# Kernel optimization log

Hardware: AMD Instinct MI355X
Metric: run time of the kernel (lower is better)

## Reference

```python
import jax, jax.numpy as jnp
import numpy as np

N, E, G = 50000, 200000, 2000        # nodes, directed edges, graphs in batch
F_IN, HID, HEADS = 64, 128, 4
DM = HID * HEADS                      # 512, concat GAT output dim
EPS = 1e-5
NEG_SLOPE = 0.2                       # PyG GATConv LeakyReLU slope


def setup_inputs() -> dict:
    key = jax.random.key(0)
    ks = jax.random.split(key, 40)
    rn = lambda k, s, sc: jax.random.normal(k, s, jnp.float32) * sc
    inp = {}
    inp["x"] = rn(ks[0], (N, F_IN), 1.0)
    inp["edge_index"] = jax.random.randint(ks[1], (2, E), 0, N)
    inp["batch"] = jnp.sort(jax.random.randint(ks[2], (N,), 0, G))
    dims = [F_IN, DM, DM]
    for l in range(3):
        d = dims[l]
        inp["W%d" % l] = rn(ks[3 + 4 * l], (d, DM), 1.0 / np.sqrt(d))
        inp["as%d" % l] = rn(ks[4 + 4 * l], (HEADS, HID), 0.1)
        inp["ad%d" % l] = rn(ks[5 + 4 * l], (HEADS, HID), 0.1)
        inp["b%d" % l] = jnp.zeros((DM,), jnp.float32)
        inp["g%d" % l] = jnp.ones((DM,), jnp.float32)
        inp["be%d" % l] = jnp.zeros((DM,), jnp.float32)
    inp["c1w"] = rn(ks[20], (2 * DM, HID), 1.0 / np.sqrt(2 * DM))
    inp["c1b"] = jnp.zeros((HID,), jnp.float32)
    inp["c2w"] = rn(ks[21], (HID, HID // 2), 1.0 / np.sqrt(HID))
    inp["c2b"] = jnp.zeros((HID // 2,), jnp.float32)
    inp["c3w"] = rn(ks[22], (HID // 2, 1), 1.0 / np.sqrt(HID // 2))
    inp["c3b"] = jnp.zeros((1,), jnp.float32)
    return inp


def _gat(x, src, dst, W, a_s, a_d, b):
    """PyG GATConv (heads=HEADS, concat) with self-loops already in src/dst."""
    n = x.shape[0]
    h = (x @ W).reshape(n, HEADS, HID)                     # [N,H,D]
    s_src = jnp.sum(h * a_s, -1)                           # [N,H]
    s_dst = jnp.sum(h * a_d, -1)                           # [N,H]
    e = jax.nn.leaky_relu(s_src[src] + s_dst[dst], NEG_SLOPE)  # [Et,H]
    # segment softmax over incoming edges of each dst node (stable)
    m = jax.lax.stop_gradient(jax.ops.segment_max(e, dst, num_segments=n))
    ex = jnp.exp(e - m[dst])
    alpha = ex / jax.ops.segment_sum(ex, dst, num_segments=n)[dst]
    out = jax.ops.segment_sum(h[src] * alpha[:, :, None], dst, num_segments=n)
    return out.reshape(n, HEADS * HID) + b


def _bn(x, g, b):
    mu = jnp.mean(x, 0)
    var = jnp.var(x, 0)
    return (x - mu) * jax.lax.rsqrt(var + EPS) * g + b


def _forward(x, edge_index, batch, layers, c1w, c1b, c2w, c2b, c3w, c3b):
    loops = jnp.arange(N)
    src = jnp.concatenate([edge_index[0], loops])          # add self-loops
    dst = jnp.concatenate([edge_index[1], loops])
    for (W, a_s, a_d, b, g, be) in layers:
        x = jax.nn.relu(_bn(_gat(x, src, dst, W, a_s, a_d, b), g, be))
    cnt = jax.ops.segment_sum(jnp.ones((N,), x.dtype), batch, num_segments=G)
    mean = jax.ops.segment_sum(x, batch, num_segments=G) / jnp.maximum(cnt, 1.0)[:, None]
    mx = jax.ops.segment_max(x, batch, num_segments=G)
    mx = jnp.where(cnt[:, None] > 0, mx, 0.0)
    h = jnp.concatenate([mean, mx], 1)                     # [G, 2*DM]
    h = jax.nn.relu(h @ c1w + c1b)
    h = jax.nn.relu(h @ c2w + c2b)
    return jax.nn.sigmoid(h @ c3w + c3b).squeeze(-1)       # [G]


def reference(x, edge_index, batch, W0, as0, ad0, b0, g0, be0, W1, as1, ad1, b1, g1, be1, W2, as2, ad2, b2, g2, be2, c1w, c1b, c2w, c2b, c3w, c3b):
    layers = [(W0, as0, ad0, b0, g0, be0), (W1, as1, ad1, b1, g1, be1), (W2, as2, ad2, b2, g2, be2)]
    return _forward(x, edge_index, batch, layers, c1w, c1b, c2w, c2b, c3w, c3b)
```

## Files before the change

kernel.cpp:

```cpp
#include <hip/hip_runtime.h>

#define N_NODES 50000
#define E_EDGES 200000
#define ET_EDGES (E_EDGES + N_NODES)
#define G_GRAPHS 2000
#define F_IN 64
#define HID 128
#define HEADS 4
#define DM 512
#define BN_EPS 1e-5f
#define NEG_SLOPE 0.2f
#define YBLK 391
#define NCHUNK (YBLK / 8)

typedef unsigned short ushort_t;
typedef float floatx4 __attribute__((ext_vector_type(4)));
typedef short short8 __attribute__((ext_vector_type(8)));

__device__ __forceinline__ float b2f(unsigned int u) {
    union { unsigned int i; float f; } v; v.i = u << 16; return v.f;
}
__device__ __forceinline__ ushort_t f2b(float f) {
    union { float f; unsigned int i; } v; v.f = f;
    unsigned int r = v.i + 0x7FFFu + ((v.i >> 16) & 1u);
    return (ushort_t)(r >> 16);
}
__device__ __forceinline__ void unpack8(uint4 v, float* f) {
    f[0] = b2f(v.x & 0xffffu); f[1] = b2f(v.x >> 16);
    f[2] = b2f(v.y & 0xffffu); f[3] = b2f(v.y >> 16);
    f[4] = b2f(v.z & 0xffffu); f[5] = b2f(v.z >> 16);
    f[6] = b2f(v.w & 0xffffu); f[7] = b2f(v.w >> 16);
}
__device__ __forceinline__ void glds16(const ushort_t* g, ushort_t* l) {
    __builtin_amdgcn_global_load_lds(
        (const __attribute__((address_space(1))) unsigned int*)g,
        (__attribute__((address_space(3))) unsigned int*)l, 16, 0, 0);
}

#define XN (N_NODES * F_IN)
#define W0N (F_IN * DM)
#define W1N (DM * DM)
__global__ __launch_bounds__(256) void k_prep(const float* __restrict__ x,
                                              const float* __restrict__ w0,
                                              const float* __restrict__ w1,
                                              const float* __restrict__ w2,
                                              ushort_t* __restrict__ Xb,
                                              ushort_t* __restrict__ Wh0,
                                              ushort_t* __restrict__ Wh1,
                                              ushort_t* __restrict__ Wh2) {
    int t = blockIdx.x * 256 + threadIdx.x;
    if (t < XN) { Xb[t] = f2b(x[t]); return; }
    t -= XN;
    if (t < W0N) {
        int k = t >> 9, n = t & 511;
        Wh0[(size_t)n * F_IN + k] = f2b(w0[t]);
        return;
    }
    t -= W0N;
    if (t < W1N) {
        int k = t >> 9, n = t & 511;
        Wh1[(size_t)n * DM + k] = f2b(w1[t]);
        return;
    }
    t -= W1N;
    if (t < W1N) {
        int k = t >> 9, n = t & 511;
        Wh2[(size_t)n * DM + k] = f2b(w2[t]);
    }
}

__global__ __launch_bounds__(256) void k_mgemm(const ushort_t* __restrict__ A,
                                               const ushort_t* __restrict__ Bh,
                                               const float* __restrict__ a_s,
                                               const float* __restrict__ a_d,
                                               ushort_t* __restrict__ C,
                                               float* __restrict__ ssrc,
                                               float* __restrict__ sdst,
                                               int M, int K) {
    __shared__ __align__(16) ushort_t Ash[128 * 32];
    __shared__ __align__(16) ushort_t Bsh[128 * 32];
    __shared__ float sS[128], sD[128];
    int bid = blockIdx.x;
    int head, yb;
    if (bid < NCHUNK * 32) {
        int chunk = bid >> 5, pos = bid & 31;
        yb = chunk * 8 + (pos & 7);
        head = pos >> 3;
    } else {
        int rem = bid - NCHUNK * 32;
        head = rem & 3;
        yb = NCHUNK * 8 + (rem >> 2);
    }
    int m0 = yb * 128, n0 = head * 128;
    int tid = threadIdx.x;
    int lane = tid & 63, wave = tid >> 6;
    int wm = (wave >> 1) * 64, wn = (wave & 1) * 64;
    floatx4 acc[4][4] = {};
    if (tid < 128) { sS[tid] = 0.f; sD[tid] = 0.f; }
    int lrow = lane >> 2, lchunk = lane & 3;
    int fs = (lrow & 3) ^ ((lrow >> 2) & 3);
    int schunk = lchunk ^ fs;
    int ar0 = wave * 16 + lrow;
    int ar1 = ar0 + 64;
    int gr0 = m0 + ar0; if (gr0 >= M) gr0 = M - 1;
    int gr1 = m0 + ar1; if (gr1 >= M) gr1 = M - 1;
    const ushort_t* gA0 = A + (size_t)gr0 * K + schunk * 8;
    const ushort_t* gA1 = A + (size_t)gr1 * K + schunk * 8;
    const ushort_t* gB0 = Bh + (size_t)(n0 + ar0) * K + schunk * 8;
    const ushort_t* gB1 = Bh + (size_t)(n0 + ar1) * K + schunk * 8;
    ushort_t* lA0 = &Ash[(wave * 16) * 32];
    ushort_t* lA1 = &Ash[(wave * 16 + 64) * 32];
    ushort_t* lB0 = &Bsh[(wave * 16) * 32];
    ushort_t* lB1 = &Bsh[(wave * 16 + 64) * 32];
    int rF = lane & 15, q = lane >> 4;
    int swz = ((q ^ (rF & 3) ^ ((rF >> 2) & 3))) * 8;
    for (int k0 = 0; k0 < K; k0 += 32) {
        glds16(gA0 + k0, lA0);
        glds16(gA1 + k0, lA1);
        glds16(gB0 + k0, lB0);
        glds16(gB1 + k0, lB1);
        __syncthreads();
        short8 af[4], bf[4];
#pragma unroll
        for (int i = 0; i < 4; ++i)
            af[i] = *(const short8*)&Ash[(wm + i * 16 + rF) * 32 + swz];
#pragma unroll
        for (int j = 0; j < 4; ++j)
            bf[j] = *(const short8*)&Bsh[(wn + j * 16 + rF) * 32 + swz];
#pragma unroll
        for (int i = 0; i < 4; ++i)
#pragma unroll
            for (int j = 0; j < 4; ++j)
                acc[i][j] = __builtin_amdgcn_mfma_f32_16x16x32_bf16(af[i], bf[j], acc[i][j], 0, 0, 0);
        __syncthreads();
    }
    int cr = (lane >> 4) * 4, cc = lane & 15;
#pragma unroll
    for (int i = 0; i < 4; ++i) {
#pragma unroll
        for (int r = 0; r < 4; ++r) {
            int gr = m0 + wm + i * 16 + cr + r;
            if (gr < M) {
#pragma unroll
                for (int j = 0; j < 4; ++j)
                    C[(size_t)gr * DM + n0 + wn + j * 16 + cc] = f2b(acc[i][j][r]);
            }
        }
    }
    float asl_[4], adl_[4];
#pragma unroll
    for (int j = 0; j < 4; ++j) {
        int c = wn + j * 16 + cc;
        asl_[j] = a_s[head * HID + c];
        adl_[j] = a_d[head * HID + c];
    }
#pragma unroll
    for (int i = 0; i < 4; ++i) {
#pragma unroll
        for (int r = 0; r < 4; ++r) {
            float ps = 0.f, pd = 0.f;
#pragma unroll
            for (int j = 0; j < 4; ++j) {
                ps += acc[i][j][r] * asl_[j];
                pd += acc[i][j][r] * adl_[j];
            }
#pragma unroll
            for (int mk = 1; mk < 16; mk <<= 1) {
                ps += __shfl_xor(ps, mk);
                pd += __shfl_xor(pd, mk);
            }
            if (cc == 0) {
                int row = wm + i * 16 + (lane >> 4) * 4 + r;
                atomicAdd(&sS[row], ps);
                atomicAdd(&sD[row], pd);
            }
        }
    }
    __syncthreads();
    if (tid < 128) {
        int gr = m0 + tid;
        if (gr < M) {
            ssrc[gr * 4 + head] = sS[tid];
            sdst[gr * 4 + head] = sD[tid];
        }
    }
}

__global__ __launch_bounds__(256) void k_bnapply(const ushort_t* __restrict__ X,
                                                 const float* __restrict__ stat,
                                                 const float* __restrict__ gam,
                                                 const float* __restrict__ bet,
                                                 ushort_t* __restrict__ Y) {
    __shared__ float sc[512], sh[512];
    int t = threadIdx.x;
    for (int f = t; f < 512; f += 256) {
        float mu = stat[f] * (1.f / (float)N_NODES);
        float var = fmaxf(stat[512 + f] * (1.f / (float)N_NODES) - mu * mu, 0.f);
        float rs = rsqrtf(var + BN_EPS);
        float s = gam[f] * rs;
        sc[f] = s;
        sh[f] = bet[f] - mu * s;
    }
    __syncthreads();
    int c8 = (t & 63) * 8;
    const float* scp = sc + c8;
    const float* shp = sh + c8;
    for (int n = blockIdx.x * 4 + (t >> 6); n < N_NODES; n += gridDim.x * 4) {
        uint4 v = *(const uint4*)&X[(size_t)n * DM + c8];
        float fv[8]; unpack8(v, fv);
        uint4 ov; unsigned* po = (unsigned*)&ov;
#pragma unroll
        for (int j = 0; j < 4; ++j) {
            unsigned lo = f2b(fmaxf(fv[2 * j] * scp[2 * j] + shp[2 * j], 0.f));
            unsigned hi = f2b(fmaxf(fv[2 * j + 1] * scp[2 * j + 1] + shp[2 * j + 1], 0.f));
            po[j] = lo | (hi << 16);
        }
        *(uint4*)&Y[(size_t)n * DM + c8] = ov;
    }
}

__global__ void k_degree(const int* __restrict__ ei, int* __restrict__ deg) {
    int e = blockIdx.x * blockDim.x + threadIdx.x;
    if (e >= ET_EDGES) return;
    int d = (e < E_EDGES) ? ei[E_EDGES + e] : (e - E_EDGES);
    atomicAdd(&deg[d], 1);
}

__global__ __launch_bounds__(1024) void k_scan3(const int* __restrict__ deg,
                                                int* __restrict__ offs,
                                                int* __restrict__ cursor) {
    __shared__ int wsum[16];
    __shared__ int carry;
    int t = threadIdx.x;
    int lane = t & 63, wv = t >> 6;
    if (t == 0) carry = 0;
    __syncthreads();
    for (int base = 0; base < N_NODES; base += 1024) {
        int i = base + t;
        int v = (i < N_NODES) ? deg[i] : 0;
        int x = v;
#pragma unroll
        for (int off = 1; off < 64; off <<= 1) {
            int y = __shfl_up(x, off);
            if (lane >= off) x += y;
        }
        if (lane == 63) wsum[wv] = x;
        __syncthreads();
        int wpre = 0;
#pragma unroll
        for (int w = 0; w < 16; ++w) wpre += (w < wv) ? wsum[w] : 0;
        int incl = wpre + x;
        if (i < N_NODES) { int o = carry + (incl - v); offs[i] = o; cursor[i] = o; }
        __syncthreads();
        if (t == 1023) carry += incl;
        __syncthreads();
    }
    if (t == 0) offs[N_NODES] = carry;
}

__global__ void k_scatter(const int* __restrict__ ei, int* __restrict__ cursor,
                          int* __restrict__ csr_src) {
    int e = blockIdx.x * blockDim.x + threadIdx.x;
    if (e >= ET_EDGES) return;
    int sv, d;
    if (e < E_EDGES) { sv = ei[e]; d = ei[E_EDGES + e]; } else { sv = d = e - E_EDGES; }
    int pos = atomicAdd(&cursor[d], 1);
    csr_src[pos] = sv;
}

__global__ void k_gbounds(const int* __restrict__ batch, int* __restrict__ gstart) {
    int i = blockIdx.x * blockDim.x + threadIdx.x;
    if (i >= N_NODES) return;
    int b = batch[i];
    int p = (i == 0) ? -1 : batch[i - 1];
    for (int g = p + 1; g <= b; ++g) gstart[g] = i;
    if (i == N_NODES - 1)
        for (int g = b + 1; g <= G_GRAPHS; ++g) gstart[g] = N_NODES;
}

__global__ __launch_bounds__(256) void k_aggregate(const ushort_t* __restrict__ H,
                                                   const float* __restrict__ ssrc,
                                                   const float* __restrict__ sdst,
                                                   const int* __restrict__ offs,
                                                   const int* __restrict__ csr_src,
                                                   const float* __restrict__ bias,
                                                   ushort_t* __restrict__ out) {
    int wave = threadIdx.x >> 6, lane = threadIdx.x & 63;
    int n = blockIdx.x * 4 + wave;
    if (n >= N_NODES) return;
    int beg = offs[n], end = offs[n + 1];
    int hl = lane >> 4, li = lane & 15;
    float sdh = sdst[n * 4 + hl];
    float m = -1e30f, s = 0.f;
    for (int e = beg + li; e < end; e += 16) {
        float sc = ssrc[csr_src[e] * 4 + hl] + sdh;
        sc = sc > 0.f ? sc : NEG_SLOPE * sc;
        if (sc > m) { s = s * __expf(m - sc) + 1.f; m = sc; }
        else s += __expf(sc - m);
    }
#pragma unroll
    for (int mk = 1; mk < 16; mk <<= 1) {
        float om = __shfl_xor(m, mk), os = __shfl_xor(s, mk);
        float mn = fmaxf(m, om);
        s = s * __expf(m - mn) + os * __expf(om - mn);
        m = mn;
    }
    float mh = m, inv = 1.f / s;
    float acc[8] = { 0.f, 0.f, 0.f, 0.f, 0.f, 0.f, 0.f, 0.f };
    int e = beg;
    for (; e + 4 <= end; e += 4) {
        int sv0 = csr_src[e], sv1 = csr_src[e + 1];
        int sv2 = csr_src[e + 2], sv3 = csr_src[e + 3];
        float s0 = ssrc[sv0 * 4 + hl], s1 = ssrc[sv1 * 4 + hl];
        float s2 = ssrc[sv2 * 4 + hl], s3 = ssrc[sv3 * 4 + hl];
        uint4 h0 = *(const uint4*)&H[(size_t)sv0 * DM + lane * 8];
        uint4 h1 = *(const uint4*)&H[(size_t)sv1 * DM + lane * 8];
        uint4 h2 = *(const uint4*)&H[(size_t)sv2 * DM + lane * 8];
        uint4 h3 = *(const uint4*)&H[(size_t)sv3 * DM + lane * 8];
        s0 += sdh; s0 = s0 > 0.f ? s0 : NEG_SLOPE * s0;
        s1 += sdh; s1 = s1 > 0.f ? s1 : NEG_SLOPE * s1;
        s2 += sdh; s2 = s2 > 0.f ? s2 : NEG_SLOPE * s2;
        s3 += sdh; s3 = s3 > 0.f ? s3 : NEG_SLOPE * s3;
        float a0 = __expf(s0 - mh) * inv, a1 = __expf(s1 - mh) * inv;
        float a2 = __expf(s2 - mh) * inv, a3 = __expf(s3 - mh) * inv;
        float f0[8], f1[8], f2[8], f3[8];
        unpack8(h0, f0); unpack8(h1, f1); unpack8(h2, f2); unpack8(h3, f3);
#pragma unroll
        for (int j = 0; j < 8; ++j)
            acc[j] += a0 * f0[j] + a1 * f1[j] + a2 * f2[j] + a3 * f3[j];
    }
    for (; e < end; ++e) {
        int sv = csr_src[e];
        float sc = ssrc[sv * 4 + hl] + sdh;
        sc = sc > 0.f ? sc : NEG_SLOPE * sc;
        float alpha = __expf(sc - mh) * inv;
        uint4 hv = *(const uint4*)&H[(size_t)sv * DM + lane * 8];
        float f[8]; unpack8(hv, f);
#pragma unroll
        for (int j = 0; j < 8; ++j) acc[j] += alpha * f[j];
    }
    const float* bp = bias + lane * 8;
    float4 b0 = *(const float4*)bp;
    float4 b1 = *(const float4*)(bp + 4);
    acc[0] += b0.x; acc[1] += b0.y; acc[2] += b0.z; acc[3] += b0.w;
    acc[4] += b1.x; acc[5] += b1.y; acc[6] += b1.z; acc[7] += b1.w;
    uint4 ov; unsigned* po = (unsigned*)&ov;
#pragma unroll
    for (int j = 0; j < 4; ++j)
        po[j] = (unsigned)f2b(acc[2 * j]) | ((unsigned)f2b(acc[2 * j + 1]) << 16);
    *(uint4*)&out[(size_t)n * DM + lane * 8] = ov;
}

#define BN_ROWS 125
__global__ __launch_bounds__(256) void k_bnstats(const ushort_t* __restrict__ X,
                                                 float* __restrict__ stat) {
    int t = threadIdx.x;
    int c2 = t * 2;
    int beg = blockIdx.x * BN_ROWS;
    int end = beg + BN_ROWS; if (end > N_NODES) end = N_NODES;
    float s0 = 0.f, s1 = 0.f, q0 = 0.f, q1 = 0.f;
    for (int n = beg; n < end; ++n) {
        unsigned v = *(const unsigned*)&X[(size_t)n * DM + c2];
        float x0 = b2f(v & 0xffffu), x1 = b2f(v >> 16);
        s0 += x0; s1 += x1;
        q0 += x0 * x0; q1 += x1 * x1;
    }
    atomicAdd(&stat[c2], s0);
    atomicAdd(&stat[c2 + 1], s1);
    atomicAdd(&stat[512 + c2], q0);
    atomicAdd(&stat[512 + c2 + 1], q1);
}

__global__ __launch_bounds__(64) void k_pool(const ushort_t* __restrict__ X,
                                             const int* __restrict__ gstart,
                                             const float* __restrict__ stat,
                                             const float* __restrict__ gam,
                                             const float* __restrict__ bet,
                                             float* __restrict__ pool) {
    int g = blockIdx.x, t = threadIdx.x;
    int beg = gstart[g], end = gstart[g + 1];
    float sc[8], sh[8];
#pragma unroll
    for (int j = 0; j < 8; ++j) {
        int f = t * 8 + j;
        float mu = stat[f] * (1.f / (float)N_NODES);
        float var = fmaxf(stat[512 + f] * (1.f / (float)N_NODES) - mu * mu, 0.f);
        float rs = rsqrtf(var + BN_EPS);
        sc[j] = gam[f] * rs;
        sh[j] = bet[f] - mu * sc[j];
    }
    float sum[8] = { 0 }, mx[8];
#pragma unroll
    for (int j = 0; j < 8; ++j) mx[j] = -1e30f;
    for (int nn = beg; nn < end; ++nn) {
        uint4 xv = *(const uint4*)&X[(size_t)nn * DM + t * 8];
        float f[8]; unpack8(xv, f);
#pragma unroll
        for (int j = 0; j < 8; ++j) {
            f[j] = fmaxf(f[j] * sc[j] + sh[j], 0.f);
            sum[j] += f[j]; mx[j] = fmaxf(mx[j], f[j]);
        }
    }
    float cnt = (float)(end - beg);
    float inv = cnt > 0.f ? 1.f / cnt : 0.f;
#pragma unroll
    for (int j = 0; j < 8; ++j) {
        pool[(size_t)g * 1024 + t * 8 + j] = sum[j] * inv;
        pool[(size_t)g * 1024 + 512 + t * 8 + j] = cnt > 0.f ? mx[j] : 0.f;
    }
}

__global__ __launch_bounds__(256) void k_mlp(const float* __restrict__ pool,
                                             const float* __restrict__ c1w,
                                             const float* __restrict__ c1b,
                                             const float* __restrict__ c2w,
                                             const float* __restrict__ c2b,
                                             const float* __restrict__ c3w,
                                             const float* __restrict__ c3b,
                                             float* __restrict__ out) {
    __shared__ float row[1024];
    __shared__ float part[128];
    __shared__ float h1[128];
    __shared__ float h2[64];
    int g = blockIdx.x, t = threadIdx.x;
    for (int i = t; i < 1024; i += 256) row[i] = pool[(size_t)g * 1024 + i];
    __syncthreads();
    int half = t >> 7, c = t & 127;
    int k0 = half * 512;
    float a1 = 0.f;
#pragma unroll 8
    for (int k = 0; k < 512; ++k) a1 += row[k0 + k] * c1w[(k0 + k) * 128 + c];
    if (half) part[c] = a1;
    __syncthreads();
    if (!half) h1[c] = fmaxf(a1 + part[c] + c1b[c], 0.f);
    __syncthreads();
    if (t < 64) {
        float a2 = c2b[t];
#pragma unroll 8
        for (int k = 0; k < 128; ++k) a2 += h1[k] * c2w[k * 64 + t];
        h2[t] = fmaxf(a2, 0.f);
    }
    __syncthreads();
    if (t < 64) {
        float p = h2[t] * c3w[t];
#pragma unroll
        for (int off = 32; off > 0; off >>= 1) p += __shfl_down(p, off);
        if (t == 0) {
            float z = p + c3b[0];
            out[g] = 1.f / (1.f + __expf(-z));
        }
    }
}

extern "C" void kernel_launch(void* const* d_in, const int* in_sizes, int n_in,
                              void* d_out, int out_size, void* d_ws, size_t ws_size,
                              hipStream_t stream) {
    const float* x = (const float*)d_in[0];
    const int* ei = (const int*)d_in[1];
    const int* batch = (const int*)d_in[2];
    const float* c1w = (const float*)d_in[21];
    const float* c1b = (const float*)d_in[22];
    const float* c2w = (const float*)d_in[23];
    const float* c2b = (const float*)d_in[24];
    const float* c3w = (const float*)d_in[25];
    const float* c3b = (const float*)d_in[26];

    char* p = (char*)d_ws;
    auto carve = [&](size_t bytes) -> char* {
        char* r = p; p += (bytes + 255) & ~(size_t)255; return r;
    };
    ushort_t* buf0   = (ushort_t*)carve((size_t)N_NODES * DM * 2);
    ushort_t* buf1   = (ushort_t*)carve((size_t)N_NODES * DM * 2);
    ushort_t* Xb     = (ushort_t*)carve((size_t)N_NODES * F_IN * 2);
    ushort_t* Wh0    = (ushort_t*)carve((size_t)F_IN * DM * 2);
    ushort_t* Wh1    = (ushort_t*)carve((size_t)DM * DM * 2);
    ushort_t* Wh2    = (ushort_t*)carve((size_t)DM * DM * 2);
    float*    ssrc   = (float*)carve((size_t)N_NODES * 4 * 4);
    float*    sdst   = (float*)carve((size_t)N_NODES * 4 * 4);
    int*      deg    = (int*)carve((size_t)N_NODES * 4);
    int*      offs   = (int*)carve((size_t)(N_NODES + 1) * 4);
    int*      cursor = (int*)carve((size_t)N_NODES * 4);
    int*      csrsrc = (int*)carve((size_t)ET_EDGES * 4);
    float*    bnstat = (float*)carve(3 * 1024 * 4);
    int*      gstart = (int*)carve((size_t)(G_GRAPHS + 1) * 4);
    float*    pool   = (float*)carve((size_t)G_GRAPHS * 1024 * 4);

    hipMemsetAsync(deg, 0, (size_t)N_NODES * 4, stream);
    hipMemsetAsync(bnstat, 0, 3 * 1024 * 4, stream);
    k_degree<<<(ET_EDGES + 255) / 256, 256, 0, stream>>>(ei, deg);
    k_scan3<<<1, 1024, 0, stream>>>(deg, offs, cursor);
    k_scatter<<<(ET_EDGES + 255) / 256, 256, 0, stream>>>(ei, cursor, csrsrc);
    k_gbounds<<<(N_NODES + 255) / 256, 256, 0, stream>>>(batch, gstart);
    {
        int total = XN + W0N + 2 * W1N;
        k_prep<<<(total + 255) / 256, 256, 0, stream>>>(
            x, (const float*)d_in[3], (const float*)d_in[9], (const float*)d_in[15],
            Xb, Wh0, Wh1, Wh2);
    }

    const ushort_t* Whs[3] = { Wh0, Wh1, Wh2 };
    const float* pgam = nullptr;
    const float* pbet = nullptr;
    const ushort_t* in = Xb;
    for (int l = 0; l < 3; ++l) {
        int K = (l == 0) ? F_IN : DM;
        const float* as_ = (const float*)d_in[4 + 6 * l];
        const float* ad_ = (const float*)d_in[5 + 6 * l];
        const float* bia = (const float*)d_in[6 + 6 * l];
        const float* gam = (const float*)d_in[7 + 6 * l];
        const float* bet = (const float*)d_in[8 + 6 * l];
        ushort_t* h   = (l % 2 == 0) ? buf1 : buf0;
        ushort_t* agg = (l % 2 == 0) ? buf0 : buf1;

        k_mgemm<<<4 * YBLK, 256, 0, stream>>>(
            in, Whs[l], as_, ad_, h, ssrc, sdst, N_NODES, K);
        k_aggregate<<<(N_NODES + 3) / 4, 256, 0, stream>>>(h, ssrc, sdst, offs, csrsrc, bia, agg);
        k_bnstats<<<(N_NODES + BN_ROWS - 1) / BN_ROWS, 256, 0, stream>>>(agg, bnstat + l * 1024);
        if (l < 2)
            k_bnapply<<<2048, 256, 0, stream>>>(agg, bnstat + l * 1024, gam, bet, h);
        in = h;
        pgam = gam; pbet = bet;
    }
    k_pool<<<G_GRAPHS, 64, 0, stream>>>(buf0, gstart, bnstat + 2 * 1024, pgam, pbet, pool);
    k_mlp<<<G_GRAPHS, 256, 0, stream>>>(pool, c1w, c1b, c2w, c2b, c3w, c3b,
                                        (float*)d_out);
}
```

Baseline: 717.7 us.

## Fold attention vectors into weights and double-buffer LDS in GAT GEMM

A new prep kernel precomputes W·a_src and W·a_dst per head in bf16. The GEMM then gets the attention scores from one extra MFMA per row tile, which replaces the shuffle-reduction and shared-memory atomic epilogue. The GEMM main loop also moves to double-buffered LDS staging, so the next K-slice loads while the current one is multiplied, with one barrier per iteration. The trade-offs are slightly lower score precision from the bf16-rounded folded weights, doubled LDS use, and a small extra launch.

Measured after the change: 705.3 us. About the same (-1.7%).

```diff
diff --git a/kernel.cpp b/kernel.cpp
--- a/kernel.cpp
+++ b/kernel.cpp
@@ -69,17 +69,44 @@
     }
 }
 
+__global__ __launch_bounds__(256) void k_wsprep(const float* __restrict__ w0,
+                                                const float* __restrict__ as0, const float* __restrict__ ad0,
+                                                const float* __restrict__ w1,
+                                                const float* __restrict__ as1, const float* __restrict__ ad1,
+                                                const float* __restrict__ w2,
+                                                const float* __restrict__ as2, const float* __restrict__ ad2,
+                                                ushort_t* __restrict__ ws0,
+                                                ushort_t* __restrict__ ws1,
+                                                ushort_t* __restrict__ ws2) {
+    int b = blockIdx.x;
+    int l = b >> 3, h = (b >> 1) & 3, v = b & 1;
+    const float* w = l == 0 ? w0 : l == 1 ? w1 : w2;
+    const float* a = v == 0 ? (l == 0 ? as0 : l == 1 ? as1 : as2)
+                            : (l == 0 ? ad0 : l == 1 ? ad1 : ad2);
+    ushort_t* o = l == 0 ? ws0 : l == 1 ? ws1 : ws2;
+    int K = l == 0 ? F_IN : DM;
+    __shared__ float av[HID];
+    int t = threadIdx.x;
+    if (t < HID) av[t] = a[h * HID + t];
+    __syncthreads();
+    for (int k = t; k < K; k += 256) {
+        const float* wr = w + (size_t)k * DM + h * HID;
+        float s = 0.f;
+#pragma unroll 8
+        for (int c = 0; c < HID; ++c) s += wr[c] * av[c];
+        o[(h * 2 + v) * K + k] = f2b(s);
+    }
+}
+
 __global__ __launch_bounds__(256) void k_mgemm(const ushort_t* __restrict__ A,
                                                const ushort_t* __restrict__ Bh,
-                                               const float* __restrict__ a_s,
-                                               const float* __restrict__ a_d,
+                                               const ushort_t* __restrict__ ws,
                                                ushort_t* __restrict__ C,
                                                float* __restrict__ ssrc,
                                                float* __restrict__ sdst,
                                                int M, int K) {
-    __shared__ __align__(16) ushort_t Ash[128 * 32];
-    __shared__ __align__(16) ushort_t Bsh[128 * 32];
-    __shared__ float sS[128], sD[128];
+    __shared__ __align__(16) ushort_t Ash[2][128 * 32];
+    __shared__ __align__(16) ushort_t Bsh[2][128 * 32];
     int bid = blockIdx.x;
     int head, yb;
     if (bid < NCHUNK * 32) {
@@ -96,7 +123,7 @@
     int lane = tid & 63, wave = tid >> 6;
     int wm = (wave >> 1) * 64, wn = (wave & 1) * 64;
     floatx4 acc[4][4] = {};
-    if (tid < 128) { sS[tid] = 0.f; sD[tid] = 0.f; }
+    floatx4 sacc[4] = {};
     int lrow = lane >> 2, lchunk = lane & 3;
     int fs = (lrow & 3) ^ ((lrow >> 2) & 3);
     int schunk = lchunk ^ fs;
@@ -108,31 +135,37 @@
     const ushort_t* gA1 = A + (size_t)gr1 * K + schunk * 8;
     const ushort_t* gB0 = Bh + (size_t)(n0 + ar0) * K + schunk * 8;
     const ushort_t* gB1 = Bh + (size_t)(n0 + ar1) * K + schunk * 8;
-    ushort_t* lA0 = &Ash[(wave * 16) * 32];
-    ushort_t* lA1 = &Ash[(wave * 16 + 64) * 32];
-    ushort_t* lB0 = &Bsh[(wave * 16) * 32];
-    ushort_t* lB1 = &Bsh[(wave * 16 + 64) * 32];
     int rF = lane & 15, q = lane >> 4;
     int swz = ((q ^ (rF & 3) ^ ((rF >> 2) & 3))) * 8;
+    const ushort_t* wsp = ws + (size_t)(head * 2 + (rF & 1)) * K + q * 8;
+    auto STAGE = [&](int b, int koff) {
+        glds16(gA0 + koff, &Ash[b][(wave * 16) * 32]);
+        glds16(gA1 + koff, &Ash[b][(wave * 16 + 64) * 32]);
+        glds16(gB0 + koff, &Bsh[b][(wave * 16) * 32]);
+        glds16(gB1 + koff, &Bsh[b][(wave * 16 + 64) * 32]);
+    };
+    STAGE(0, 0);
+    __syncthreads();
+    int cur = 0;
     for (int k0 = 0; k0 < K; k0 += 32) {
-        glds16(gA0 + k0, lA0);
-        glds16(gA1 + k0, lA1);
-        glds16(gB0 + k0, lB0);
-        glds16(gB1 + k0, lB1);
-        __syncthreads();
+        if (k0 + 32 < K) STAGE(cur ^ 1, k0 + 32);
+        short8 sf = *(const short8*)&wsp[k0];
         short8 af[4], bf[4];
 #pragma unroll
         for (int i = 0; i < 4; ++i)
-            af[i] = *(const short8*)&Ash[(wm + i * 16 + rF) * 32 + swz];
+            af[i] = *(const short8*)&Ash[cur][(wm + i * 16 + rF) * 32 + swz];
 #pragma unroll
         for (int j = 0; j < 4; ++j)
-            bf[j] = *(const short8*)&Bsh[(wn + j * 16 + rF) * 32 + swz];
-#pragma unroll
-        for (int i = 0; i < 4; ++i)
+            bf[j] = *(const short8*)&Bsh[cur][(wn + j * 16 + rF) * 32 + swz];
+#pragma unroll
+        for (int i = 0; i < 4; ++i) {
+            sacc[i] = __builtin_amdgcn_mfma_f32_16x16x32_bf16(af[i], sf, sacc[i], 0, 0, 0);
 #pragma unroll
             for (int j = 0; j < 4; ++j)
                 acc[i][j] = __builtin_amdgcn_mfma_f32_16x16x32_bf16(af[i], bf[j], acc[i][j], 0, 0, 0);
+        }
         __syncthreads();
+        cur ^= 1;
     }
     int cr = (lane >> 4) * 4, cc = lane & 15;
 #pragma unroll
@@ -144,44 +177,9 @@
 #pragma unroll
                 for (int j = 0; j < 4; ++j)
                     C[(size_t)gr * DM + n0 + wn + j * 16 + cc] = f2b(acc[i][j][r]);
+                if (cc == 0) ssrc[gr * 4 + head] = sacc[i][r];
+                else if (cc == 1) sdst[gr * 4 + head] = sacc[i][r];
             }
-        }
-    }
-    float asl_[4], adl_[4];
-#pragma unroll
-    for (int j = 0; j < 4; ++j) {
-        int c = wn + j * 16 + cc;
-        asl_[j] = a_s[head * HID + c];
-        adl_[j] = a_d[head * HID + c];
-    }
-#pragma unroll
-    for (int i = 0; i < 4; ++i) {
-#pragma unroll
-        for (int r = 0; r < 4; ++r) {
-            float ps = 0.f, pd = 0.f;
-#pragma unroll
-            for (int j = 0; j < 4; ++j) {
-                ps += acc[i][j][r] * asl_[j];
-                pd += acc[i][j][r] * adl_[j];
-            }
-#pragma unroll
-            for (int mk = 1; mk < 16; mk <<= 1) {
-                ps += __shfl_xor(ps, mk);
-                pd += __shfl_xor(pd, mk);
-            }
-            if (cc == 0) {
-                int row = wm + i * 16 + (lane >> 4) * 4 + r;
-                atomicAdd(&sS[row], ps);
-                atomicAdd(&sD[row], pd);
-            }
-        }
-    }
-    __syncthreads();
-    if (tid < 128) {
-        int gr = m0 + tid;
-        if (gr < M) {
-            ssrc[gr * 4 + head] = sS[tid];
-            sdst[gr * 4 + head] = sD[tid];
         }
     }
 }
@@ -475,6 +473,9 @@
     ushort_t* Wh0    = (ushort_t*)carve((size_t)F_IN * DM * 2);
     ushort_t* Wh1    = (ushort_t*)carve((size_t)DM * DM * 2);
     ushort_t* Wh2    = (ushort_t*)carve((size_t)DM * DM * 2);
+    ushort_t* ws0    = (ushort_t*)carve((size_t)8 * F_IN * 2);
+    ushort_t* ws1    = (ushort_t*)carve((size_t)8 * DM * 2);
+    ushort_t* ws2    = (ushort_t*)carve((size_t)8 * DM * 2);
     float*    ssrc   = (float*)carve((size_t)N_NODES * 4 * 4);
     float*    sdst   = (float*)carve((size_t)N_NODES * 4 * 4);
     int*      deg    = (int*)carve((size_t)N_NODES * 4);
@@ -497,15 +498,19 @@
             x, (const float*)d_in[3], (const float*)d_in[9], (const float*)d_in[15],
             Xb, Wh0, Wh1, Wh2);
     }
+    k_wsprep<<<24, 256, 0, stream>>>(
+        (const float*)d_in[3], (const float*)d_in[4], (const float*)d_in[5],
+        (const float*)d_in[9], (const float*)d_in[10], (const float*)d_in[11],
+        (const float*)d_in[15], (const float*)d_in[16], (const float*)d_in[17],
+        ws0, ws1, ws2);
 
     const ushort_t* Whs[3] = { Wh0, Wh1, Wh2 };
+    const ushort_t* wss[3] = { ws0, ws1, ws2 };
     const float* pgam = nullptr;
     const float* pbet = nullptr;
     const ushort_t* in = Xb;
     for (int l = 0; l < 3; ++l) {
         int K = (l == 0) ? F_IN : DM;
-        const float* as_ = (const float*)d_in[4 + 6 * l];
-        const float* ad_ = (const float*)d_in[5 + 6 * l];
         const float* bia = (const float*)d_in[6 + 6 * l];
         const float* gam = (const float*)d_in[7 + 6 * l];
         const float* bet = (const float*)d_in[8 + 6 * l];
@@ -513,7 +518,7 @@
         ushort_t* agg = (l % 2 == 0) ? buf0 : buf1;
 
         k_mgemm<<<4 * YBLK, 256, 0, stream>>>(
-            in, Whs[l], as_, ad_, h, ssrc, sdst, N_NODES, K);
+            in, Whs[l], wss[l], h, ssrc, sdst, N_NODES, K);
         k_aggregate<<<(N_NODES + 3) / 4, 256, 0, stream>>>(h, ssrc, sdst, offs, csrsrc, bia, agg);
         k_bnstats<<<(N_NODES + BN_ROWS - 1) / BN_ROWS, 256, 0, stream>>>(agg, bnstat + l * 1024);
         if (l < 2)
```
